# Kernel optimization log

Measured on AMD Instinct MI355X. Metric: run time of the kernel, lower is better.

## Reference

```python
import jax, jax.numpy as jnp
import numpy as np

N_QUBITS = 12
N_LAYERS = 6
BATCH = 512
DIM = 2 ** N_QUBITS


def _apply_1q(psi, G, wire):
    """Apply a single-qubit gate on `wire` (wire 0 = most significant).
    psi: [B, 2^n] complex. G: [2,2] (shared) or [B,2,2] (batched)."""
    B = psi.shape[0]
    left = 2 ** wire
    psi = psi.reshape(B, left, 2, -1)
    if G.ndim == 2:
        psi = jnp.einsum('ij,bxjy->bxiy', G, psi)
    else:
        psi = jnp.einsum('bij,bxjy->bxiy', G, psi)
    return psi.reshape(B, -1)


def _apply_cnot(psi, c, t):
    """CNOT with control c, target t on [B, 2^n] state."""
    B = psi.shape[0]
    ps = psi.reshape((B,) + (2,) * N_QUBITS)
    ca, ta = c + 1, t + 1
    c0 = jnp.take(ps, 0, axis=ca)
    c1 = jnp.take(ps, 1, axis=ca)
    flip_ax = ta if ta < ca else ta - 1
    c1 = jnp.flip(c1, axis=flip_ax)  # X on target within control=1 block
    ps = jnp.stack([c0, c1], axis=ca)
    return ps.reshape(B, -1)


def _circuit(x, weights):
    B = x.shape[0]
    psi = jnp.zeros((B, DIM), jnp.complex64).at[:, 0].set(1.0)

    # AngleEmbedding: RY(x_w) on each wire (batched gate matrices)
    h = 0.5 * x
    c, s = jnp.cos(h).astype(jnp.complex64), jnp.sin(h).astype(jnp.complex64)
    for w in range(N_QUBITS):
        G = jnp.stack([jnp.stack([c[:, w], -s[:, w]], -1),
                       jnp.stack([s[:, w], c[:, w]], -1)], -2)  # [B,2,2]
        psi = _apply_1q(psi, G, w)

    # StronglyEntanglingLayers: Rot(phi,theta,omega) per wire, then ring of CNOTs
    for l in range(N_LAYERS):
        phi, theta, omega = weights[l, :, 0], weights[l, :, 1], weights[l, :, 2]
        ct = jnp.cos(0.5 * theta).astype(jnp.complex64)
        st = jnp.sin(0.5 * theta).astype(jnp.complex64)
        ep = jnp.exp(-0.5j * (phi + omega).astype(jnp.complex64))
        em = jnp.exp(0.5j * (phi - omega).astype(jnp.complex64))
        # Rot = RZ(omega) RY(theta) RZ(phi)
        m00 = ep * ct
        m01 = -em * st
        m10 = jnp.conj(em) * st
        m11 = jnp.conj(ep) * ct
        for w in range(N_QUBITS):
            G = jnp.array([[m00[w], m01[w]], [m10[w], m11[w]]], jnp.complex64)
            psi = _apply_1q(psi, G, w)
        r = l % (N_QUBITS - 1) + 1
        for w in range(N_QUBITS):
            psi = _apply_cnot(psi, w, (w + r) % N_QUBITS)

    # <Z_w> for every wire
    probs = psi.real ** 2 + psi.imag ** 2  # [B, 2^n]
    exps = []
    for w in range(N_QUBITS):
        p = probs.reshape(B, 2 ** w, 2, -1)
        exps.append(p[:, :, 0, :].sum((1, 2)) - p[:, :, 1, :].sum((1, 2)))
    return jnp.stack(exps, -1)  # [B, n_qubits]


def setup_inputs() -> dict:
    key = jax.random.key(0)
    k1, k2, k3, k4 = jax.random.split(key, 4)
    x = jax.random.uniform(k1, (BATCH, N_QUBITS), jnp.float32, -np.pi, np.pi)
    weights = jax.random.uniform(k2, (N_LAYERS, N_QUBITS, 3), jnp.float32, 0.0, 2.0 * np.pi)
    W = jax.random.normal(k3, (1, N_QUBITS), jnp.float32) * 0.3
    b = jax.random.normal(k4, (1,), jnp.float32) * 0.01
    return {"x": x, "weights": weights, "W": W, "b": b}


def reference(x, weights, W, b):
    z = _circuit(x, weights)              # [B, n_qubits]
    y = z @ W.T + b                       # [B, 1]
    return y.squeeze(-1)                  # [B]
```

## Files before the change

### kernel.cpp

```cpp
#include <hip/hip_runtime.h>
#include <stdint.h>

#define NQ 12
#define DIM 4096
#define NLAYERS 6
#define TPB 256

struct CK_t {
    uint32_t SM[NLAYERS][NQ];
    uint32_t frow[NQ];
};

constexpr uint32_t slotmap(uint32_t k) { return ((k & 15u) << 8) | (k >> 4); }

constexpr CK_t build_ck() {
    CK_t ck{};
    uint32_t Mcol[NQ];
    for (int q = 0; q < NQ; q++) Mcol[q] = 1u << q;
    for (int l = 0; l < NLAYERS; l++) {
        for (int q = 0; q < NQ; q++) ck.SM[l][q] = slotmap(Mcol[q]);
        int r = l % (NQ - 1) + 1;
        uint32_t Acol[NQ]{}, Aicol[NQ]{};
        for (int q = 0; q < NQ; q++) {
            uint32_t v = 1u << q;
            for (int w = NQ - 1; w >= 0; w--) {
                int pc = NQ - 1 - w, pt = NQ - 1 - ((w + r) % NQ);
                v ^= ((v >> pc) & 1u) << pt;
            }
            Acol[q] = v;
            uint32_t u = 1u << q;
            for (int w = 0; w < NQ; w++) {
                int pc = NQ - 1 - w, pt = NQ - 1 - ((w + r) % NQ);
                u ^= ((u >> pc) & 1u) << pt;
            }
            Aicol[q] = u;
        }
        for (int q = 0; q < NQ; q++) Mcol[q] = Acol[q];
        if (l == NLAYERS - 1) {
            for (int p = 0; p < NQ; p++) {
                uint32_t s = 0;
                for (int q = 0; q < NQ; q++) s |= ((Aicol[q] >> p) & 1u) << q;
                ck.frow[p] = s;
            }
        }
    }
    return ck;
}
constexpr CK_t CK = build_ck();

__device__ __forceinline__ float sxor(float v, uint32_t s) {
    return __uint_as_float(__float_as_uint(v) ^ s);
}

template<int L>
__device__ __forceinline__ void do_pass(float (&RE)[16], float (&IM)[16],
                                        const float4* smat, float2* xb, int tid) {
    float2* buf = xb + ((L & 1) ? DIM : 0);
    float2* wrow = buf + tid;
    #pragma unroll
    for (int l = 0; l < 16; l++) wrow[l << 8] = make_float2(RE[l], IM[l]);

    float4 m1 = smat[L * NQ + 1];
    float4 m0 = smat[L * NQ + 0];
    uint32_t sa = (uint32_t)((tid >> 6) & 1) << 31;
    uint32_t sb = (uint32_t)((tid >> 7) & 1) << 31;
    float A0r = m1.x,           A0i = sxor(m1.y, sa);
    float A1r = sxor(m1.z, sa), A1i = m1.w;
    float B0r = m0.x,           B0i = sxor(m0.y, sb);
    float B1r = sxor(m0.z, sb), B1i = m0.w;
    float c00r = A0r*B0r - A0i*B0i, c00i = A0r*B0i + A0i*B0r;
    float c01r = A0r*B1r - A0i*B1i, c01i = A0r*B1i + A0i*B1r;
    float c10r = A1r*B0r - A1i*B0i, c10i = A1r*B0i + A1i*B0r;
    float c11r = A1r*B1r - A1i*B1i, c11i = A1r*B1i + A1i*B1r;

    uint32_t srcT = 0;
    #pragma unroll
    for (int j = 0; j < 8; j++)
        srcT ^= ((tid >> j) & 1) ? CK.SM[L][4 + j] : 0u;

    __syncthreads();

    #pragma unroll
    for (int l = 0; l < 16; l++) {
        uint32_t C00 = 0;
        #pragma unroll
        for (int q = 0; q < 4; q++)
            if ((l >> q) & 1) C00 ^= CK.SM[L][q];
        uint32_t i00 = srcT ^ C00;
        uint32_t i10 = i00 ^ CK.SM[L][10];
        uint32_t i01 = i00 ^ CK.SM[L][11];
        uint32_t i11 = i10 ^ CK.SM[L][11];
        float2 s00 = buf[i00], s10 = buf[i10], s01 = buf[i01], s11 = buf[i11];
        float nr = c00r*s00.x - c00i*s00.y;
        float ni = c00r*s00.y + c00i*s00.x;
        nr += c10r*s10.x - c10i*s10.y;  ni += c10r*s10.y + c10i*s10.x;
        nr += c01r*s01.x - c01i*s01.y;  ni += c01r*s01.y + c01i*s01.x;
        nr += c11r*s11.x - c11i*s11.y;  ni += c11r*s11.y + c11i*s11.x;
        RE[l] = nr; IM[l] = ni;
    }
}

template<int L, int W>
__device__ __forceinline__ void lane_gate(float (&RE)[16], float (&IM)[16],
                                          const float4* smat, int tid) {
    constexpr int q  = NQ - 1 - W;
    constexpr int lm = 1 << (q - 4);
    float4 m = smat[L * NQ + W];
    uint32_t sgn = (uint32_t)((tid >> (q - 4)) & 1) << 31;
    float fai = sxor(m.y, sgn), fbr = sxor(m.z, sgn);
    #pragma unroll
    for (int l = 0; l < 16; l++) {
        float orr = __shfl_xor(RE[l], lm, 64);
        float oii = __shfl_xor(IM[l], lm, 64);
        float nr = m.x*RE[l] - fai*IM[l] + fbr*orr - m.w*oii;
        float ni = m.x*IM[l] + fai*RE[l] + fbr*oii + m.w*orr;
        RE[l] = nr; IM[l] = ni;
    }
}

template<int L, int W>
__device__ __forceinline__ void reg_gate(float (&RE)[16], float (&IM)[16],
                                         const float4* smat) {
    constexpr int q = NQ - 1 - W;
    float4 m = smat[L * NQ + W];
    #pragma unroll
    for (int l = 0; l < 16; l++) {
        if (l & (1 << q)) continue;
        int l2 = l | (1 << q);
        float a0r = RE[l], a0i = IM[l], a1r = RE[l2], a1i = IM[l2];
        RE[l]  = m.x*a0r - m.y*a0i + m.z*a1r - m.w*a1i;
        IM[l]  = m.x*a0i + m.y*a0r + m.z*a1i + m.w*a1r;
        RE[l2] = m.x*a1r + m.y*a1i - m.z*a0r - m.w*a0i;
        IM[l2] = m.x*a1i - m.y*a1r - m.z*a0i + m.w*a0r;
    }
}

template<int L>
__device__ __forceinline__ void do_layer(float (&RE)[16], float (&IM)[16],
                                         const float4* smat, float2* xb, int tid) {
    do_pass<L>(RE, IM, smat, xb, tid);
    lane_gate<L, 2>(RE, IM, smat, tid);
    lane_gate<L, 3>(RE, IM, smat, tid);
    lane_gate<L, 4>(RE, IM, smat, tid);
    lane_gate<L, 5>(RE, IM, smat, tid);
    lane_gate<L, 6>(RE, IM, smat, tid);
    lane_gate<L, 7>(RE, IM, smat, tid);
    reg_gate<L, 8>(RE, IM, smat);
    reg_gate<L, 9>(RE, IM, smat);
    reg_gate<L, 10>(RE, IM, smat);
    reg_gate<L, 11>(RE, IM, smat);
}

__global__ __launch_bounds__(TPB) void qsim_kernel(
    const float* __restrict__ x,
    const float* __restrict__ weights,
    const float* __restrict__ Wp,
    const float* __restrict__ bptr,
    float* __restrict__ out)
{
    __shared__ float2 xb[2 * DIM];
    __shared__ float4 smat[NLAYERS * NQ];
    __shared__ float  scs[NQ], sss[NQ];
    __shared__ float  red[4];

    const int tid = threadIdx.x;
    const int b   = blockIdx.x;

    if (tid < NQ) {
        float s_, c_;
        sincosf(0.5f * x[b * NQ + tid], &s_, &c_);
        scs[tid] = c_; sss[tid] = s_;
    }
    if (tid < NLAYERS * NQ) {
        float phi   = weights[tid * 3 + 0];
        float theta = weights[tid * 3 + 1];
        float omega = weights[tid * 3 + 2];
        float st, ct; sincosf(0.5f * theta, &st, &ct);
        float sp, cp; sincosf(0.5f * (phi + omega), &sp, &cp);
        float sm, cm; sincosf(0.5f * (phi - omega), &sm, &cm);
        smat[tid] = make_float4(cp * ct, -sp * ct, -cm * st, -sm * st);
    }
    __syncthreads();

    float base = 1.0f;
    #pragma unroll
    for (int p = 4; p < NQ; p++) {
        int w = NQ - 1 - p;
        base *= ((tid >> (p - 4)) & 1) ? sss[w] : scs[w];
    }
    float RE[16], IM[16];
    #pragma unroll
    for (int l = 0; l < 16; l++) {
        float a = base;
        #pragma unroll
        for (int p = 0; p < 4; p++) {
            int w = NQ - 1 - p;
            a *= ((l >> p) & 1) ? sss[w] : scs[w];
        }
        RE[l] = a; IM[l] = 0.0f;
    }

    do_layer<0>(RE, IM, smat, xb, tid);
    do_layer<1>(RE, IM, smat, xb, tid);
    do_layer<2>(RE, IM, smat, xb, tid);
    do_layer<3>(RE, IM, smat, xb, tid);
    do_layer<4>(RE, IM, smat, xb, tid);
    do_layer<5>(RE, IM, smat, xb, tid);

    const float bv = bptr[0];
    float wb[NQ];
    #pragma unroll
    for (int p = 0; p < NQ; p++) {
        uint32_t row = CK.frow[p];
        int tp = __popc(tid & (int)(row >> 4)) & 1;
        float Wv = Wp[NQ - 1 - p];
        wb[p] = tp ? -Wv : Wv;
    }
    float acc = 0.0f;
    #pragma unroll
    for (int l = 0; l < 16; l++) {
        float coef = bv;
        #pragma unroll
        for (int p = 0; p < NQ; p++)
            coef += (__popc(l & (int)(CK.frow[p] & 15u)) & 1) ? -wb[p] : wb[p];
        acc += (RE[l] * RE[l] + IM[l] * IM[l]) * coef;
    }
    #pragma unroll
    for (int off = 32; off > 0; off >>= 1)
        acc += __shfl_down(acc, off, 64);
    if ((tid & 63) == 0) red[tid >> 6] = acc;
    __syncthreads();
    if (tid == 0) out[b] = red[0] + red[1] + red[2] + red[3];
}

extern "C" void kernel_launch(void* const* d_in, const int* in_sizes, int n_in,
                              void* d_out, int out_size, void* d_ws, size_t ws_size,
                              hipStream_t stream) {
    const float* x       = (const float*)d_in[0];
    const float* weights = (const float*)d_in[1];
    const float* W       = (const float*)d_in[2];
    const float* bptr    = (const float*)d_in[3];
    qsim_kernel<<<512, TPB, 0, stream>>>(x, weights, W, bptr, (float*)d_out);
}
```

Before: 102.2 us.

## Replace shuffle and fused-pair gates with three LDS transposes per layer

Each layer previously did one LDS pass that applied two gates with four gathers per element, then six shuffle-based lane gates and four register gates. Now each layer does three LDS permutation passes, each followed by four in-register gates, so all gates run in registers and cross-lane shuffles disappear. The first layer's entry pass is folded into the initial product state, and the final readout masks are recomputed for the new layout. This trades about 36 DPP shuffles and extra gather loads per layer for more LDS store/load round trips and barriers.

```diff
diff --git a/kernel.cpp b/kernel.cpp
--- a/kernel.cpp
+++ b/kernel.cpp
@@ -7,148 +7,127 @@
 #define TPB 256
 
 struct CK_t {
-    uint32_t SM[NLAYERS][NQ];
+    uint32_t RC1[NLAYERS][NQ];
+    uint32_t RC2[NQ];
+    uint32_t RC3[NQ];
     uint32_t frow[NQ];
 };
 
-constexpr uint32_t slotmap(uint32_t k) { return ((k & 15u) << 8) | (k >> 4); }
+constexpr uint32_t G2f(uint32_t k){ return ((k&15u)<<8) | (k&0xF0u) | ((k>>8)&15u); }
+constexpr uint32_t G3f(uint32_t k){ return ((k&15u)<<4) | ((k>>4)&15u) | (k&0xF00u); }
+constexpr uint32_t Lstd(uint32_t k){ return ((k&15u)<<8) | (k>>4); }
+constexpr uint32_t Lpr(uint32_t k){ return ((k>>6)&15u) | (((k>>4)&3u)<<4) | (((k>>10)&3u)<<6) | ((k&15u)<<8); }
 
 constexpr CK_t build_ck() {
     CK_t ck{};
-    uint32_t Mcol[NQ];
-    for (int q = 0; q < NQ; q++) Mcol[q] = 1u << q;
+    uint32_t Acols[NLAYERS][NQ]{}, Aicol5[NQ]{};
     for (int l = 0; l < NLAYERS; l++) {
-        for (int q = 0; q < NQ; q++) ck.SM[l][q] = slotmap(Mcol[q]);
         int r = l % (NQ - 1) + 1;
-        uint32_t Acol[NQ]{}, Aicol[NQ]{};
         for (int q = 0; q < NQ; q++) {
             uint32_t v = 1u << q;
             for (int w = NQ - 1; w >= 0; w--) {
                 int pc = NQ - 1 - w, pt = NQ - 1 - ((w + r) % NQ);
                 v ^= ((v >> pc) & 1u) << pt;
             }
-            Acol[q] = v;
-            uint32_t u = 1u << q;
-            for (int w = 0; w < NQ; w++) {
-                int pc = NQ - 1 - w, pt = NQ - 1 - ((w + r) % NQ);
-                u ^= ((u >> pc) & 1u) << pt;
-            }
-            Aicol[q] = u;
-        }
-        for (int q = 0; q < NQ; q++) Mcol[q] = Acol[q];
-        if (l == NLAYERS - 1) {
-            for (int p = 0; p < NQ; p++) {
-                uint32_t s = 0;
-                for (int q = 0; q < NQ; q++) s |= ((Aicol[q] >> p) & 1u) << q;
-                ck.frow[p] = s;
+            Acols[l][q] = v;
+            if (l == NLAYERS - 1) {
+                uint32_t u = 1u << q;
+                for (int w = 0; w < NQ; w++) {
+                    int pc = NQ - 1 - w, pt = NQ - 1 - ((w + r) % NQ);
+                    u ^= ((u >> pc) & 1u) << pt;
+                }
+                Aicol5[q] = u;
             }
         }
     }
+    for (int j = 0; j < NQ; j++) ck.RC2[j] = Lstd(G2f(1u << j));
+    for (int j = 0; j < NQ; j++) ck.RC3[j] = Lpr(G3f(1u << j));
+    for (int l = 1; l < NLAYERS; l++)
+        for (int j = 0; j < NQ; j++)
+            ck.RC1[l][j] = Lstd(G3f(G2f(Acols[l - 1][j])));
+    uint32_t Mcol[NQ]{};
+    for (int j = 0; j < NQ; j++) {
+        uint32_t pj = G2f(G3f(1u << j));
+        uint32_t M = 0;
+        for (int m = 0; m < NQ; m++) if ((pj >> m) & 1u) M ^= Aicol5[m];
+        Mcol[j] = M;
+    }
+    for (int p = 0; p < NQ; p++) {
+        uint32_t s = 0;
+        for (int j = 0; j < NQ; j++) s |= ((Mcol[j] >> p) & 1u) << j;
+        ck.frow[p] = s;
+    }
     return ck;
 }
 constexpr CK_t CK = build_ck();
 
-__device__ __forceinline__ float sxor(float v, uint32_t s) {
-    return __uint_as_float(__float_as_uint(v) ^ s);
-}
-
-template<int L>
+template<int KIND, int L, int PAR>
 __device__ __forceinline__ void do_pass(float (&RE)[16], float (&IM)[16],
-                                        const float4* smat, float2* xb, int tid) {
-    float2* buf = xb + ((L & 1) ? DIM : 0);
-    float2* wrow = buf + tid;
-    #pragma unroll
-    for (int l = 0; l < 16; l++) wrow[l << 8] = make_float2(RE[l], IM[l]);
-
-    float4 m1 = smat[L * NQ + 1];
-    float4 m0 = smat[L * NQ + 0];
-    uint32_t sa = (uint32_t)((tid >> 6) & 1) << 31;
-    uint32_t sb = (uint32_t)((tid >> 7) & 1) << 31;
-    float A0r = m1.x,           A0i = sxor(m1.y, sa);
-    float A1r = sxor(m1.z, sa), A1i = m1.w;
-    float B0r = m0.x,           B0i = sxor(m0.y, sb);
-    float B1r = sxor(m0.z, sb), B1i = m0.w;
-    float c00r = A0r*B0r - A0i*B0i, c00i = A0r*B0i + A0i*B0r;
-    float c01r = A0r*B1r - A0i*B1i, c01i = A0r*B1i + A0i*B1r;
-    float c10r = A1r*B0r - A1i*B0i, c10i = A1r*B0i + A1i*B0r;
-    float c11r = A1r*B1r - A1i*B1i, c11i = A1r*B1i + A1i*B1r;
+                                        float2* xb, int tid) {
+    float2* buf = xb + PAR * DIM;
+    int wbase;
+    if constexpr (KIND == 3) wbase = (int)Lpr((uint32_t)tid << 4);
+    else                     wbase = tid;
+    #pragma unroll
+    for (int l = 0; l < 16; l++)
+        buf[wbase + (l << 8)] = make_float2(RE[l], IM[l]);
 
     uint32_t srcT = 0;
     #pragma unroll
-    for (int j = 0; j < 8; j++)
-        srcT ^= ((tid >> j) & 1) ? CK.SM[L][4 + j] : 0u;
-
+    for (int j = 0; j < 8; j++) {
+        uint32_t c = (KIND == 1) ? CK.RC1[L][4 + j]
+                   : (KIND == 2) ? CK.RC2[4 + j] : CK.RC3[4 + j];
+        srcT ^= ((tid >> j) & 1) ? c : 0u;
+    }
     __syncthreads();
-
-    #pragma unroll
-    for (int l = 0; l < 16; l++) {
-        uint32_t C00 = 0;
+    #pragma unroll
+    for (int l = 0; l < 16; l++) {
+        uint32_t C = 0;
         #pragma unroll
         for (int q = 0; q < 4; q++)
-            if ((l >> q) & 1) C00 ^= CK.SM[L][q];
-        uint32_t i00 = srcT ^ C00;
-        uint32_t i10 = i00 ^ CK.SM[L][10];
-        uint32_t i01 = i00 ^ CK.SM[L][11];
-        uint32_t i11 = i10 ^ CK.SM[L][11];
-        float2 s00 = buf[i00], s10 = buf[i10], s01 = buf[i01], s11 = buf[i11];
-        float nr = c00r*s00.x - c00i*s00.y;
-        float ni = c00r*s00.y + c00i*s00.x;
-        nr += c10r*s10.x - c10i*s10.y;  ni += c10r*s10.y + c10i*s10.x;
-        nr += c01r*s01.x - c01i*s01.y;  ni += c01r*s01.y + c01i*s01.x;
-        nr += c11r*s11.x - c11i*s11.y;  ni += c11r*s11.y + c11i*s11.x;
-        RE[l] = nr; IM[l] = ni;
-    }
-}
-
-template<int L, int W>
-__device__ __forceinline__ void lane_gate(float (&RE)[16], float (&IM)[16],
-                                          const float4* smat, int tid) {
-    constexpr int q  = NQ - 1 - W;
-    constexpr int lm = 1 << (q - 4);
-    float4 m = smat[L * NQ + W];
-    uint32_t sgn = (uint32_t)((tid >> (q - 4)) & 1) << 31;
-    float fai = sxor(m.y, sgn), fbr = sxor(m.z, sgn);
-    #pragma unroll
-    for (int l = 0; l < 16; l++) {
-        float orr = __shfl_xor(RE[l], lm, 64);
-        float oii = __shfl_xor(IM[l], lm, 64);
-        float nr = m.x*RE[l] - fai*IM[l] + fbr*orr - m.w*oii;
-        float ni = m.x*IM[l] + fai*RE[l] + fbr*oii + m.w*orr;
-        RE[l] = nr; IM[l] = ni;
-    }
-}
-
-template<int L, int W>
+            if ((l >> q) & 1)
+                C ^= (KIND == 1) ? CK.RC1[L][q]
+                   : (KIND == 2) ? CK.RC2[q] : CK.RC3[q];
+        float2 v = buf[srcT ^ C];
+        RE[l] = v.x; IM[l] = v.y;
+    }
+}
+
+template<int L, int W, int Q>
 __device__ __forceinline__ void reg_gate(float (&RE)[16], float (&IM)[16],
                                          const float4* smat) {
-    constexpr int q = NQ - 1 - W;
     float4 m = smat[L * NQ + W];
     #pragma unroll
     for (int l = 0; l < 16; l++) {
-        if (l & (1 << q)) continue;
-        int l2 = l | (1 << q);
+        if (l & (1 << Q)) continue;
+        int l2 = l | (1 << Q);
         float a0r = RE[l], a0i = IM[l], a1r = RE[l2], a1i = IM[l2];
-        RE[l]  = m.x*a0r - m.y*a0i + m.z*a1r - m.w*a1i;
-        IM[l]  = m.x*a0i + m.y*a0r + m.z*a1i + m.w*a1r;
-        RE[l2] = m.x*a1r + m.y*a1i - m.z*a0r - m.w*a0i;
-        IM[l2] = m.x*a1i - m.y*a1r - m.z*a0i + m.w*a0r;
+        RE[l]  = m.x * a0r - m.y * a0i + m.z * a1r - m.w * a1i;
+        IM[l]  = m.x * a0i + m.y * a0r + m.z * a1i + m.w * a1r;
+        RE[l2] = m.x * a1r + m.y * a1i - m.z * a0r - m.w * a0i;
+        IM[l2] = m.x * a1i - m.y * a1r - m.z * a0i + m.w * a0r;
     }
 }
 
 template<int L>
 __device__ __forceinline__ void do_layer(float (&RE)[16], float (&IM)[16],
                                          const float4* smat, float2* xb, int tid) {
-    do_pass<L>(RE, IM, smat, xb, tid);
-    lane_gate<L, 2>(RE, IM, smat, tid);
-    lane_gate<L, 3>(RE, IM, smat, tid);
-    lane_gate<L, 4>(RE, IM, smat, tid);
-    lane_gate<L, 5>(RE, IM, smat, tid);
-    lane_gate<L, 6>(RE, IM, smat, tid);
-    lane_gate<L, 7>(RE, IM, smat, tid);
-    reg_gate<L, 8>(RE, IM, smat);
-    reg_gate<L, 9>(RE, IM, smat);
-    reg_gate<L, 10>(RE, IM, smat);
-    reg_gate<L, 11>(RE, IM, smat);
+    if constexpr (L > 0)
+        do_pass<1, L, (3 * L - 1) & 1>(RE, IM, xb, tid);
+    reg_gate<L, 11, 0>(RE, IM, smat);
+    reg_gate<L, 10, 1>(RE, IM, smat);
+    reg_gate<L,  9, 2>(RE, IM, smat);
+    reg_gate<L,  8, 3>(RE, IM, smat);
+    do_pass<2, L, (3 * L) & 1>(RE, IM, xb, tid);
+    reg_gate<L, 3, 0>(RE, IM, smat);
+    reg_gate<L, 2, 1>(RE, IM, smat);
+    reg_gate<L, 1, 2>(RE, IM, smat);
+    reg_gate<L, 0, 3>(RE, IM, smat);
+    do_pass<3, L, (3 * L + 1) & 1>(RE, IM, xb, tid);
+    reg_gate<L, 7, 0>(RE, IM, smat);
+    reg_gate<L, 6, 1>(RE, IM, smat);
+    reg_gate<L, 5, 2>(RE, IM, smat);
+    reg_gate<L, 4, 3>(RE, IM, smat);
 }
 
 __global__ __launch_bounds__(TPB) void qsim_kernel(
```

Result: faster. 98.81 us (-3.3%).
